# Kernel tuning notes

Measured on AMD Instinct MI355X. Metric: run time of the kernel, lower is better.

The kernel has to match this reference:

```python
import jax, jax.numpy as jnp
import numpy as np

IN_FEATURES = 4096
OUT_FEATURES = 4096
ALPHA = 0.01  # dequant scale = input_scale * weight_scale
BETA = 1.0


def setup_inputs() -> dict:
    key = jax.random.key(0)
    kx, kw, kb = jax.random.split(key, 3)
    # int8 activations (W8A8): values in [-127, 127]
    x = jax.random.randint(kx, (4, 2048, IN_FEATURES), -127, 128, dtype=jnp.int8)
    # int8 weight buffer, [out_features, in_features] as in the torch module
    weight = jax.random.randint(kw, (OUT_FEATURES, IN_FEATURES), -127, 128, dtype=jnp.int8)
    # fp32 bias, [1, out_features]
    bias = jax.random.normal(kb, (1, OUT_FEATURES), dtype=jnp.float32)
    alpha = jnp.float32(ALPHA)
    return {"x": x, "weight": weight, "bias": bias, "alpha": alpha}


def reference(x, weight, bias, alpha):
    # y = alpha * (x_int8 @ W_int8^T) + beta * bias, accumulated in int32, output fp32
    x_shape = x.shape
    x2 = x.reshape(-1, x_shape[-1])  # [B*S, in]
    # int8 GEMM with int32 accumulation (faithful to the fused kernel's math)
    acc = jax.lax.dot_general(
        x2, weight,
        dimension_numbers=(((1,), (1,)), ((), ())),
        preferred_element_type=jnp.int32,
    )  # [B*S, out]
    y = alpha * acc.astype(jnp.float32) + BETA * bias  # fused dequant + bias
    return y.reshape(*x_shape[:-1], OUT_FEATURES)
```

## Files before the change

kernel.cpp:

```cpp
#include <hip/hip_runtime.h>
#include <stdint.h>

typedef int v4i __attribute__((ext_vector_type(4)));

constexpr int K_DIM = 4096;
constexpr int N_DIM = 4096;
constexpr int TM = 128;
constexpr int TN = 128;
constexpr int TK = 128;
constexpr int KSTEPS = K_DIM / TK;

__device__ __forceinline__ int pack4(int a, int b, int c, int d) {
    unsigned r = (unsigned(a) & 0xFFu)
               | ((unsigned(b) & 0xFFu) << 8)
               | ((unsigned(c) & 0xFFu) << 16)
               | (unsigned(d) << 24);
    return (int)r;
}

__global__ __launch_bounds__(256) void pack_both(
    const int* __restrict__ s1, int* __restrict__ d1, int n1,
    const int* __restrict__ s2, int* __restrict__ d2, int n2)
{
    int idx = blockIdx.x * blockDim.x + threadIdx.x;
    const int* s;
    int* d;
    if (idx < n1) { s = s1; d = d1; }
    else if (idx < n1 + n2) { s = s2; d = d2; idx -= n1; }
    else return;
    v4i v = ((const v4i*)s)[idx];
    d[idx] = pack4(v.x, v.y, v.z, v.w);
}

__device__ __forceinline__ void gld16(const int8_t* g, int8_t* l) {
    __builtin_amdgcn_global_load_lds(
        (const __attribute__((address_space(1))) char*)g,
        (__attribute__((address_space(3))) char*)l,
        16, 0, 0);
}

__global__ __launch_bounds__(256) void w8a8_gemm_packed(
    const int8_t* __restrict__ X,
    const int8_t* __restrict__ Wt,
    const float*  __restrict__ bias,
    const float*  __restrict__ alphap,
    float* __restrict__ Y)
{
    __shared__ __align__(16) int8_t As[TM * TK];
    __shared__ __align__(16) int8_t Bs[TN * TK];

    const int tid  = threadIdx.x;
    const int lane = tid & 63;
    const int wave = tid >> 6;

    const int m0 = blockIdx.x * TM;
    const int n0 = blockIdx.y * TN;

    const int8_t* Aga[4];
    const int8_t* Bga[4];
    int lds_off[4];
#pragma unroll
    for (int i = 0; i < 4; ++i) {
        const int c    = (wave * 4 + i) * 64 + lane;
        const int row  = c >> 3;
        const int gko  = ((c & 7) ^ ((row >> 1) & 7)) << 4;
        Aga[i] = X  + (size_t)(m0 + row) * K_DIM + gko;
        Bga[i] = Wt + (size_t)(n0 + row) * K_DIM + gko;
        lds_off[i] = c << 4;
    }

    const int wm   = (wave & 1) << 6;
    const int wn   = (wave >> 1) << 6;
    const int lrow = lane & 15;
    const int quad = lane >> 4;

    int a_off[4], b_off[4];
#pragma unroll
    for (int i = 0; i < 4; ++i) {
        const int ra = wm + i * 16 + lrow;
        a_off[i] = ra * TK + ((quad ^ ((ra >> 1) & 7)) << 4);
        const int rb = wn + i * 16 + lrow;
        b_off[i] = rb * TK + ((quad ^ ((rb >> 1) & 7)) << 4);
    }

    v4i acc[4][4] = {};

    for (int kt = 0; kt < KSTEPS; ++kt) {
        const int kb = kt * TK;
#pragma unroll
        for (int i = 0; i < 4; ++i) {
            gld16(Aga[i] + kb, As + lds_off[i]);
            gld16(Bga[i] + kb, Bs + lds_off[i]);
        }
        __syncthreads();

#pragma unroll
        for (int kk = 0; kk < 2; ++kk) {
            const int kx = kk << 6;
            v4i a[4], b[4];
#pragma unroll
            for (int i = 0; i < 4; ++i) a[i] = *(const v4i*)(As + (a_off[i] ^ kx));
#pragma unroll
            for (int j = 0; j < 4; ++j) b[j] = *(const v4i*)(Bs + (b_off[j] ^ kx));
#pragma unroll
            for (int i = 0; i < 4; ++i)
#pragma unroll
                for (int j = 0; j < 4; ++j)
                    acc[i][j] = __builtin_amdgcn_mfma_i32_16x16x64_i8(a[i], b[j], acc[i][j], 0, 0, 0);
        }

        __syncthreads();
    }

    const float alpha = *alphap;
#pragma unroll
    for (int j = 0; j < 4; ++j) {
        const int col = n0 + wn + j * 16 + lrow;
        const float bj = bias[col];
#pragma unroll
        for (int i = 0; i < 4; ++i) {
            const size_t rbase = (size_t)(m0 + wm + i * 16 + quad * 4) * N_DIM + col;
#pragma unroll
            for (int r = 0; r < 4; ++r)
                Y[rbase + (size_t)r * N_DIM] = fmaf(alpha, (float)acc[i][j][r], bj);
        }
    }
}

__global__ __launch_bounds__(256, 2) void w8a8_gemm_fb(
    const int*   __restrict__ X,
    const int*   __restrict__ Wt,
    const float* __restrict__ bias,
    const float* __restrict__ alphap,
    float* __restrict__ Y)
{
    __shared__ __align__(16) int8_t As[TM * 64];
    __shared__ __align__(16) int8_t Bs[TN * 64];

    const int tid  = threadIdx.x;
    const int lane = tid & 63;
    const int wave = tid >> 6;
    const int m0 = blockIdx.x * TM;
    const int n0 = blockIdx.y * TN;

    const int srow = tid >> 3;
    const int sk   = (tid & 7) * 8;
    const int* Ag = X  + (size_t)(m0 + srow) * K_DIM + sk;
    const int* Bg = Wt + (size_t)(n0 + srow) * K_DIM + sk;

    int wr_off[4];
#pragma unroll
    for (int r = 0; r < 4; ++r) {
        const int row = r * 32 + (tid >> 3);
        const int dw  = (tid & 7) * 2;
        const int sw  = row * 16 + (((dw >> 2) ^ ((row >> 1) & 3)) << 2) + (dw & 3);
        wr_off[r] = sw * 4;
    }

    const int wm   = (wave & 1) << 6;
    const int wn   = (wave >> 1) << 6;
    const int lrow = lane & 15;
    const int quad = lane >> 4;

    int a_off[4], b_off[4];
#pragma unroll
    for (int i = 0; i < 4; ++i) {
        const int ra = wm + i * 16 + lrow;
        a_off[i] = ra * 64 + ((quad ^ ((ra >> 1) & 3)) << 4);
        const int rb = wn + i * 16 + lrow;
        b_off[i] = rb * 64 + ((quad ^ ((rb >> 1) & 3)) << 4);
    }

    v4i acc[4][4] = {};
    v4i av[8], bv[8];
#pragma unroll
    for (int r = 0; r < 4; ++r) {
        const int* pa = Ag + (size_t)r * 32 * K_DIM;
        const int* pb = Bg + (size_t)r * 32 * K_DIM;
        av[2 * r] = *(const v4i*)(pa);  av[2 * r + 1] = *(const v4i*)(pa + 4);
        bv[2 * r] = *(const v4i*)(pb);  bv[2 * r + 1] = *(const v4i*)(pb + 4);
    }

    for (int kt = 0; kt < 64; ++kt) {
#pragma unroll
        for (int r = 0; r < 4; ++r) {
            int2 pa2, pb2;
            pa2.x = pack4(av[2*r].x,   av[2*r].y,   av[2*r].z,   av[2*r].w);
            pa2.y = pack4(av[2*r+1].x, av[2*r+1].y, av[2*r+1].z, av[2*r+1].w);
            pb2.x = pack4(bv[2*r].x,   bv[2*r].y,   bv[2*r].z,   bv[2*r].w);
            pb2.y = pack4(bv[2*r+1].x, bv[2*r+1].y, bv[2*r+1].z, bv[2*r+1].w);
            *(int2*)(As + wr_off[r]) = pa2;
            *(int2*)(Bs + wr_off[r]) = pb2;
        }
        const int kn = (kt + 1 < 64) ? (kt + 1) : kt;
        const int koff = kn * 64;
#pragma unroll
        for (int r = 0; r < 4; ++r) {
            const int* pa = Ag + (size_t)r * 32 * K_DIM + koff;
            const int* pb = Bg + (size_t)r * 32 * K_DIM + koff;
            av[2 * r] = *(const v4i*)(pa);  av[2 * r + 1] = *(const v4i*)(pa + 4);
            bv[2 * r] = *(const v4i*)(pb);  bv[2 * r + 1] = *(const v4i*)(pb + 4);
        }
        __syncthreads();
        v4i a[4], b[4];
#pragma unroll
        for (int i = 0; i < 4; ++i) a[i] = *(const v4i*)(As + a_off[i]);
#pragma unroll
        for (int j = 0; j < 4; ++j) b[j] = *(const v4i*)(Bs + b_off[j]);
#pragma unroll
        for (int i = 0; i < 4; ++i)
#pragma unroll
            for (int j = 0; j < 4; ++j)
                acc[i][j] = __builtin_amdgcn_mfma_i32_16x16x64_i8(a[i], b[j], acc[i][j], 0, 0, 0);
        __syncthreads();
    }

    const float alpha = *alphap;
#pragma unroll
    for (int j = 0; j < 4; ++j) {
        const int col = n0 + wn + j * 16 + lrow;
        const float bj = bias[col];
#pragma unroll
        for (int i = 0; i < 4; ++i) {
            const size_t rbase = (size_t)(m0 + wm + i * 16 + quad * 4) * N_DIM + col;
#pragma unroll
            for (int r = 0; r < 4; ++r)
                Y[rbase + (size_t)r * N_DIM] = fmaf(alpha, (float)acc[i][j][r], bj);
        }
    }
}

extern "C" void kernel_launch(void* const* d_in, const int* in_sizes, int n_in,
                              void* d_out, int out_size, void* d_ws, size_t ws_size,
                              hipStream_t stream) {
    const int*   X32   = (const int*)d_in[0];
    const int*   W32   = (const int*)d_in[1];
    const float* bias  = (const float*)d_in[2];
    const float* alpha = (const float*)d_in[3];
    float* Y = (float*)d_out;

    const int nX = in_sizes[0];
    const int nW = in_sizes[1];
    const int M  = nX / K_DIM;
    dim3 grid(M / TM, N_DIM / TN);

    if (ws_size >= (size_t)nX + (size_t)nW) {
        int8_t* Xp = (int8_t*)d_ws;
        int8_t* Wp = Xp + nX;
        const int n1 = nX / 4, n2 = nW / 4;
        const int nthreads = n1 + n2;
        pack_both<<<(nthreads + 255) / 256, 256, 0, stream>>>(
            X32, (int*)Xp, n1, W32, (int*)Wp, n2);
        w8a8_gemm_packed<<<grid, dim3(256), 0, stream>>>(Xp, Wp, bias, alpha, Y);
    } else {
        w8a8_gemm_fb<<<grid, dim3(256), 0, stream>>>(X32, W32, bias, alpha, Y);
    }
}
```

Baseline: 417.0 us.

## Add 256x256-tile double-buffered int8 GEMM kernel with async LDS prefetch

Adds a new 512-thread GEMM kernel for the packed path. Each block computes a 256x256 output tile from 128 KB of dynamic LDS, split into two buffers. The next K-slice is prefetched with global_load_lds: A loads are issued before compute and B loads between the two MFMA halves, with explicit vmcnt waits and raw barriers. The kernel also uses a block-index swizzle for L2 locality and s_setprio around the MFMA bursts. The aim is more data reuse per LDS byte and overlap of loads with compute. In exchange it keeps 128 accumulator registers per thread, fits only one block per CU, and its swizzle hardcodes a 32x16 block grid.

```diff
diff --git a/kernel.cpp b/kernel.cpp
--- a/kernel.cpp
+++ b/kernel.cpp
@@ -39,6 +39,128 @@
         16, 0, 0);
 }
 
+constexpr int BM = 256;
+constexpr int BN = 256;
+constexpr int BKB = 128;
+constexpr int KT = K_DIM / BKB;
+
+__global__ __launch_bounds__(512, 2) void w8a8_gemm_256(
+    const int8_t* __restrict__ X,
+    const int8_t* __restrict__ Wt,
+    const float*  __restrict__ bias,
+    const float*  __restrict__ alphap,
+    float* __restrict__ Y)
+{
+    extern __shared__ __align__(128) int8_t smem[];
+
+    const int tid  = threadIdx.x;
+    const int lane = tid & 63;
+    const int wave = tid >> 6;
+
+    const int flat = blockIdx.x;
+    const int swz  = (flat & 7) * 64 + (flat >> 3);
+    const int m0   = (swz & 31) * BM;
+    const int n0   = (swz >> 5) * BN;
+
+    int ag[4], bg[4], ldso[4];
+#pragma unroll
+    for (int q = 0; q < 4; ++q) {
+        const int c   = q * 512 + tid;
+        const int row = c >> 3;
+        const int gko = ((c & 7) ^ ((row >> 1) & 7)) << 4;
+        ag[q]   = (m0 + row) * K_DIM + gko;
+        bg[q]   = (n0 + row) * K_DIM + gko;
+        ldso[q] = c << 4;
+    }
+
+    const int wm   = (wave & 1) << 7;
+    const int wn   = (wave >> 1) << 6;
+    const int lrow = lane & 15;
+    const int quad = lane >> 4;
+
+    int a_off[8], b_off[4];
+#pragma unroll
+    for (int i = 0; i < 8; ++i) {
+        const int ra = wm + i * 16 + lrow;
+        a_off[i] = ra * BKB + ((quad ^ ((ra >> 1) & 7)) << 4);
+    }
+#pragma unroll
+    for (int j = 0; j < 4; ++j) {
+        const int rb = wn + j * 16 + lrow;
+        b_off[j] = rb * BKB + ((quad ^ ((rb >> 1) & 7)) << 4);
+    }
+
+    v4i acc[8][4] = {};
+
+#pragma unroll
+    for (int q = 0; q < 4; ++q) gld16(X  + ag[q], smem + ldso[q]);
+#pragma unroll
+    for (int q = 0; q < 4; ++q) gld16(Wt + bg[q], smem + 32768 + ldso[q]);
+
+    for (int t = 0; t < KT; ++t) {
+        int8_t* Ard = smem + ((t & 1) << 16);
+        int8_t* Brd = Ard + 32768;
+        const int kb1 = (t + 1) * BKB;
+
+        if (t + 1 < KT) {
+            int8_t* Awr = smem + (((t + 1) & 1) << 16);
+#pragma unroll
+            for (int q = 0; q < 4; ++q) gld16(X + ag[q] + kb1, Awr + ldso[q]);
+            asm volatile("s_waitcnt vmcnt(4)" ::: "memory");
+        } else {
+            asm volatile("s_waitcnt vmcnt(0)" ::: "memory");
+        }
+        asm volatile("s_barrier" ::: "memory");
+
+        v4i a[8], b[4];
+#pragma unroll
+        for (int i = 0; i < 8; ++i) a[i] = *(const v4i*)(Ard + a_off[i]);
+#pragma unroll
+        for (int j = 0; j < 4; ++j) b[j] = *(const v4i*)(Brd + b_off[j]);
+        __builtin_amdgcn_s_setprio(1);
+#pragma unroll
+        for (int i = 0; i < 8; ++i)
+#pragma unroll
+            for (int j = 0; j < 4; ++j)
+                acc[i][j] = __builtin_amdgcn_mfma_i32_16x16x64_i8(a[i], b[j], acc[i][j], 0, 0, 0);
+        __builtin_amdgcn_s_setprio(0);
+
+        if (t + 1 < KT) {
+            int8_t* Bwr = smem + (((t + 1) & 1) << 16) + 32768;
+#pragma unroll
+            for (int q = 0; q < 4; ++q) gld16(Wt + bg[q] + kb1, Bwr + ldso[q]);
+        }
+
+#pragma unroll
+        for (int i = 0; i < 8; ++i) a[i] = *(const v4i*)(Ard + (a_off[i] ^ 64));
+#pragma unroll
+        for (int j = 0; j < 4; ++j) b[j] = *(const v4i*)(Brd + (b_off[j] ^ 64));
+        __builtin_amdgcn_s_setprio(1);
+#pragma unroll
+        for (int i = 0; i < 8; ++i)
+#pragma unroll
+            for (int j = 0; j < 4; ++j)
+                acc[i][j] = __builtin_amdgcn_mfma_i32_16x16x64_i8(a[i], b[j], acc[i][j], 0, 0, 0);
+        __builtin_amdgcn_s_setprio(0);
+
+        asm volatile("s_barrier" ::: "memory");
+    }
+
+    const float alpha = *alphap;
+#pragma unroll
+    for (int j = 0; j < 4; ++j) {
+        const int col = n0 + wn + j * 16 + lrow;
+        const float bj = bias[col];
+#pragma unroll
+        for (int i = 0; i < 8; ++i) {
+            const size_t rbase = (size_t)(m0 + wm + i * 16 + quad * 4) * N_DIM + col;
+#pragma unroll
+            for (int r = 0; r < 4; ++r)
+                Y[rbase + (size_t)r * N_DIM] = fmaf(alpha, (float)acc[i][j][r], bj);
+        }
+    }
+}
+
 __global__ __launch_bounds__(256) void w8a8_gemm_packed(
     const int8_t* __restrict__ X,
     const int8_t* __restrict__ Wt,
@@ -242,7 +364,6 @@
     const int nX = in_sizes[0];
     const int nW = in_sizes[1];
     const int M  = nX / K_DIM;
-    dim3 grid(M / TM, N_DIM / TN);
 
     if (ws_size >= (size_t)nX + (size_t)nW) {
         int8_t* Xp = (int8_t*)d_ws;
@@ -251,8 +372,21 @@
         const int nthreads = n1 + n2;
         pack_both<<<(nthreads + 255) / 256, 256, 0, stream>>>(
             X32, (int*)Xp, n1, W32, (int*)Wp, n2);
-        w8a8_gemm_packed<<<grid, dim3(256), 0, stream>>>(Xp, Wp, bias, alpha, Y);
+
+        static hipError_t attr = hipFuncSetAttribute(
+            reinterpret_cast<const void*>(w8a8_gemm_256),
+            hipFuncAttributeMaxDynamicSharedMemorySize, 131072);
+
+        if (attr == hipSuccess && (M % BM) == 0) {
+            const int nblocks = (M / BM) * (N_DIM / BN);
+            w8a8_gemm_256<<<dim3(nblocks), dim3(512), 131072, stream>>>(
+                Xp, Wp, bias, alpha, Y);
+        } else {
+            dim3 grid(M / TM, N_DIM / TN);
+            w8a8_gemm_packed<<<grid, dim3(256), 0, stream>>>(Xp, Wp, bias, alpha, Y);
+        }
     } else {
+        dim3 grid(M / TM, N_DIM / TN);
         w8a8_gemm_fb<<<grid, dim3(256), 0, stream>>>(X32, W32, bias, alpha, Y);
     }
 }
```

Measured after the change: 391.6 us. 6.1% less time.
